# Performance work log

Hardware: AMD Instinct MI355X
Metric: run time of the kernel (lower is better)

The kernel has to match this reference:

```python
import jax, jax.numpy as jnp
import numpy as np

N_NODES = 50000
N_EDGES = 800000
VOCAB = 4096          # node_emb_size
EMB_DIM = 128         # node_emb_dim
HIDDEN = 128          # hidden_dim -> layer1 out = 2*HIDDEN
N_POS = 1024


def gcn_conv(h, edge_index, W, b, n):
    """PyG GCNConv: lin -> add self loops -> sym-normalized scatter-add -> +bias."""
    h = h @ W                                   # [N, out]
    row, col = edge_index[0], edge_index[1]     # source, target
    loop = jnp.arange(n)
    row = jnp.concatenate([row, loop])
    col = jnp.concatenate([col, loop])
    deg = jax.ops.segment_sum(jnp.ones(row.shape[0], dtype=h.dtype), col, num_segments=n)
    dinv = jnp.where(deg > 0, jax.lax.rsqrt(deg), 0.0)
    norm = dinv[row] * dinv[col]                # [E+N]
    msg = h[row] * norm[:, None]                # gather + scale
    return jax.ops.segment_sum(msg, col, num_segments=n) + b


def setup_inputs() -> dict:
    key = jax.random.key(0)
    ks = jax.random.split(key, 10)
    x = jax.random.randint(ks[0], (N_NODES, 1), 0, VOCAB)
    edge_index = jax.random.randint(ks[1], (2, N_EDGES), 0, N_NODES)
    x_position = jax.random.randint(ks[2], (N_POS,), 0, N_NODES)
    # Embedding init: normal(0, emb_dim^-0.5) per initialize_parameters
    emb = jax.random.normal(ks[3], (VOCAB, EMB_DIM), jnp.float32) * EMB_DIM ** -0.5
    # GCN / linear weights (glorot-ish)
    W1 = jax.random.normal(ks[4], (EMB_DIM, 2 * HIDDEN), jnp.float32) * (EMB_DIM ** -0.5)
    b1 = jnp.zeros((2 * HIDDEN,), jnp.float32)
    W2 = jax.random.normal(ks[5], (2 * HIDDEN, HIDDEN), jnp.float32) * ((2 * HIDDEN) ** -0.5)
    b2 = jnp.zeros((HIDDEN,), jnp.float32)
    Wc = jax.random.normal(ks[6], (HIDDEN, VOCAB), jnp.float32) * (HIDDEN ** -0.5)
    bc = jnp.zeros((VOCAB,), jnp.float32)
    return {"x": x, "edge_index": edge_index, "x_position": x_position,
            "emb": emb, "W1": W1, "b1": b1, "W2": W2, "b2": b2, "Wc": Wc, "bc": bc}


def reference(x, edge_index, x_position, emb, W1, b1, W2, b2, Wc, bc):
    n = x.shape[0]
    h = emb[x[:, 0]]                                   # Embedding + squeeze(1)
    h = jax.nn.relu(gcn_conv(h, edge_index, W1, b1, n))
    z = gcn_conv(h, edge_index, W2, b2, n)             # [N, HIDDEN]
    logits = z @ Wc + bc                               # classifier over all nodes
    # embedding stage: mean of classified rows at x_position, keep dim 0
    return jnp.mean(logits[x_position], axis=0, keepdims=True)  # [1, VOCAB]
```

## Files before the change

kernel.cpp:

```cpp
#include <hip/hip_runtime.h>

constexpr int EMB  = 128;
constexpr int H1D  = 256;
constexpr int H2D  = 128;
constexpr int VOC  = 4096;
constexpr int NSL  = 32;

__global__ void k_init(int* cnt, int* count, float* wsum, int* nflag, int* total, int n) {
    int i = blockIdx.x * blockDim.x + threadIdx.x;
    if (i < n) { cnt[i] = 0; count[i] = 0; }
    if (i < NSL * H1D) wsum[i] = 0.0f;
    if (i == 0) { *nflag = 0; *total = 0; }
}

__global__ void k_histcnt(const int* __restrict__ col, const int* __restrict__ xpos,
                          int* cnt, int* count, int ne, int np) {
    int e = blockIdx.x * blockDim.x + threadIdx.x;
    if (e < ne) atomicAdd(&cnt[col[e]], 1);
    if (e < np) atomicAdd(&count[xpos[e]], 1);
}

__global__ void k_waggE(const int* __restrict__ row, const int* __restrict__ col,
                        const int* __restrict__ count, const int* __restrict__ cnt,
                        float* wagg, int ne) {
    int e = blockIdx.x * blockDim.x + threadIdx.x;
    if (e < ne) {
        int c = col[e];
        int cc = count[c];
        if (cc > 0) {
            int r = row[e];
            float dc = rsqrtf((float)cnt[c] + 1.0f);
            float dr = rsqrtf((float)cnt[r] + 1.0f);
            atomicAdd(&wagg[r], (float)cc * dc * dr);
        }
    }
}

__global__ void k_alloc(float* wagg, const int* __restrict__ cnt,
                        const int* __restrict__ count,
                        int* needlist, int* nflag, int* total,
                        int* offs, int* cursor, int n) {
    int v = blockIdx.x * blockDim.x + threadIdx.x;
    int lane = threadIdx.x & 63;
    float wa = 0.0f;
    int cv = 0;
    bool need = false;
    if (v < n) {
        wa = wagg[v];
        int cc = count[v];
        cv = cnt[v];
        if (cc > 0) {
            float d2 = 1.0f / ((float)cv + 1.0f);
            wa += (float)cc * d2;
        }
        need = (wa > 0.0f);
        if (need) wagg[v] = wa;
    }
    int seg = need ? cv : 0;
    int incl = seg;
#pragma unroll
    for (int d = 1; d < 64; d <<= 1) {
        int t = __shfl_up(incl, d);
        if (lane >= d) incl += t;
    }
    int excl = incl - seg;
    int wave_total = __shfl(incl, 63);
    unsigned long long mask = __ballot(need);
    int rank = __popcll(mask & ((1ull << lane) - 1));
    int wcnt = __popcll(mask);
    int base_id = 0, base_off = 0;
    if (lane == 0) {
        if (wcnt > 0) base_id = atomicAdd(nflag, wcnt);
        if (wave_total > 0) base_off = atomicAdd(total, wave_total);
    }
    base_id  = __shfl(base_id, 0);
    base_off = __shfl(base_off, 0);
    if (need) {
        needlist[base_id + rank] = v;
        int o = base_off + excl;
        offs[v] = o;
        cursor[v] = o;
    }
}

__global__ void k_scatter(const int* __restrict__ row, const int* __restrict__ col,
                          const float* __restrict__ wagg, const int* __restrict__ x,
                          const int* __restrict__ cnt,
                          int* cursor, int* srowx, float* srowd, int ne) {
    int e = blockIdx.x * blockDim.x + threadIdx.x;
    if (e < ne) {
        int c = col[e];
        if (wagg[c] > 0.0f) {
            int r = row[e];
            int pos = atomicAdd(&cursor[c], 1);
            srowx[pos] = x[r];
            srowd[pos] = rsqrtf((float)cnt[r] + 1.0f);
        }
    }
}

constexpr int RPB = 16;
__global__ void k_embW1(const float* __restrict__ emb, const float* __restrict__ W1,
                        float* __restrict__ embW1) {
    __shared__ float er[RPB][EMB];
    int t = threadIdx.x;
    int r0 = blockIdx.x * RPB;
    for (int i = t; i < RPB * EMB; i += 256) {
        er[i / EMB][i % EMB] = emb[(size_t)r0 * EMB + i];
    }
    __syncthreads();
    float acc[RPB];
#pragma unroll
    for (int rr = 0; rr < RPB; rr++) acc[rr] = 0.0f;
    for (int k = 0; k < EMB; k++) {
        float w = W1[k * H1D + t];
#pragma unroll
        for (int rr = 0; rr < RPB; rr++) acc[rr] += er[rr][k] * w;
    }
#pragma unroll
    for (int rr = 0; rr < RPB; rr++) {
        embW1[(size_t)(r0 + rr) * H1D + t] = acc[rr];
    }
}

__global__ void k_fconv(const int* __restrict__ needlist, const int* __restrict__ nneed_p,
                        const float* __restrict__ wagg, const int* __restrict__ x,
                        const int* __restrict__ srowx, const float* __restrict__ srowd,
                        const int* __restrict__ offs, const int* __restrict__ cnt,
                        const float* __restrict__ embW1, const float* __restrict__ b1,
                        float* __restrict__ wsum) {
    int lane = threadIdx.x & 63;
    int wib  = threadIdx.x >> 6;
    int wid  = blockIdx.x * (blockDim.x >> 6) + wib;
    int nw   = gridDim.x * (blockDim.x >> 6);
    int nn   = *nneed_p;
    const float4* __restrict__ ew = (const float4*)embW1;
    float4 bfrag = ((const float4*)b1)[lane];
    float4 acc2 = {0.0f, 0.0f, 0.0f, 0.0f};

    for (int i = wid; i < nn; i += nw) {
        int v = needlist[i];
        int cv = cnt[v];
        float dv = rsqrtf((float)cv + 1.0f);
        float wa = wagg[v];
        float4 s = ew[(size_t)x[v] * 64 + lane];
        float w0 = dv * dv;
        float4 acc;
        acc.x = bfrag.x + w0 * s.x;
        acc.y = bfrag.y + w0 * s.y;
        acc.z = bfrag.z + w0 * s.z;
        acc.w = bfrag.w + w0 * s.w;
        int start = offs[v], m = cv;
        for (int base = 0; base < m; base += 64) {
            int mm = min(64, m - base);
            int xr = 0; float wr = 0.0f;
            if (lane < mm) {
                xr = srowx[start + base + lane];
                wr = srowd[start + base + lane] * dv;
            }
            int e = 0;
            for (; e + 4 <= mm; e += 4) {
                int i0 = __shfl(xr, e),     i1 = __shfl(xr, e + 1);
                int i2 = __shfl(xr, e + 2), i3 = __shfl(xr, e + 3);
                float q0 = __shfl(wr, e),     q1 = __shfl(wr, e + 1);
                float q2 = __shfl(wr, e + 2), q3 = __shfl(wr, e + 3);
                float4 t0 = ew[(size_t)i0 * 64 + lane];
                float4 t1 = ew[(size_t)i1 * 64 + lane];
                float4 t2 = ew[(size_t)i2 * 64 + lane];
                float4 t3 = ew[(size_t)i3 * 64 + lane];
                acc.x += q0 * t0.x + q1 * t1.x + q2 * t2.x + q3 * t3.x;
                acc.y += q0 * t0.y + q1 * t1.y + q2 * t2.y + q3 * t3.y;
                acc.z += q0 * t0.z + q1 * t1.z + q2 * t2.z + q3 * t3.z;
                acc.w += q0 * t0.w + q1 * t1.w + q2 * t2.w + q3 * t3.w;
            }
            for (; e < mm; e++) {
                int i0 = __shfl(xr, e);
                float q0 = __shfl(wr, e);
                float4 t0 = ew[(size_t)i0 * 64 + lane];
                acc.x += q0 * t0.x;
                acc.y += q0 * t0.y;
                acc.z += q0 * t0.z;
                acc.w += q0 * t0.w;
            }
        }
        acc2.x += wa * fmaxf(acc.x, 0.0f);
        acc2.y += wa * fmaxf(acc.y, 0.0f);
        acc2.z += wa * fmaxf(acc.z, 0.0f);
        acc2.w += wa * fmaxf(acc.w, 0.0f);
    }

    __shared__ float red[4][H1D];
    red[wib][4 * lane + 0] = acc2.x;
    red[wib][4 * lane + 1] = acc2.y;
    red[wib][4 * lane + 2] = acc2.z;
    red[wib][4 * lane + 3] = acc2.w;
    __syncthreads();
    int t = threadIdx.x;
    float ssum = red[0][t] + red[1][t] + red[2][t] + red[3][t];
    atomicAdd(&wsum[(blockIdx.x & (NSL - 1)) * H1D + t], ssum);
}

__global__ void k_zout(const float* __restrict__ wsum, const float* __restrict__ W2,
                       const float* __restrict__ b2, const float* __restrict__ Wc,
                       const float* __restrict__ bc, float* __restrict__ out,
                       float inv_np) {
    __shared__ float ws[H1D];
    __shared__ float z[H2D];
    int t = threadIdx.x;
    float s = 0.0f;
#pragma unroll
    for (int c = 0; c < NSL; c++) s += wsum[c * H1D + t];
    ws[t] = s;
    __syncthreads();
    if (t < H2D) {
        float acc = 0.0f;
#pragma unroll 8
        for (int k = 0; k < H1D; k++) acc += ws[k] * W2[k * H2D + t];
        z[t] = b2[t] + acc * inv_np;
    }
    __syncthreads();
    int c = blockIdx.x * blockDim.x + t;
    float acc = bc[c];
#pragma unroll 8
    for (int j = 0; j < H2D; j++) acc += z[j] * Wc[(size_t)j * VOC + c];
    out[c] = acc;
}

extern "C" void kernel_launch(void* const* d_in, const int* in_sizes, int n_in,
                              void* d_out, int out_size, void* d_ws, size_t ws_size,
                              hipStream_t stream) {
    const int n  = in_sizes[0];
    const int ne = in_sizes[1] / 2;
    const int np = in_sizes[2];

    const int*   x    = (const int*)d_in[0];
    const int*   ei   = (const int*)d_in[1];
    const int*   xpos = (const int*)d_in[2];
    const float* emb  = (const float*)d_in[3];
    const float* W1   = (const float*)d_in[4];
    const float* b1   = (const float*)d_in[5];
    const float* W2   = (const float*)d_in[6];
    const float* b2   = (const float*)d_in[7];
    const float* Wc   = (const float*)d_in[8];
    const float* bc   = (const float*)d_in[9];
    float*       out  = (float*)d_out;

    const int* row = ei;
    const int* col = ei + ne;

    char* p = (char*)d_ws;
    auto alloc = [&](size_t bytes) {
        char* r = p;
        p += (bytes + 255) & ~(size_t)255;
        return r;
    };
    int*   cnt      = (int*)alloc((size_t)n * 4);
    int*   offs     = (int*)alloc((size_t)n * 4);
    int*   cursor   = (int*)alloc((size_t)n * 4);
    int*   count    = (int*)alloc((size_t)n * 4);
    int*   needlist = (int*)alloc((size_t)n * 4);
    int*   srowx    = (int*)alloc((size_t)ne * 4);
    float* srowd    = (float*)alloc((size_t)ne * 4);
    int*   nflag    = (int*)alloc(256 * 4);
    int*   total    = (int*)alloc(256 * 4);
    float* wagg     = (float*)alloc((size_t)n * 4);
    float* embW1    = (float*)alloc((size_t)VOC * H1D * 4);
    float* wsum     = (float*)alloc((size_t)NSL * H1D * 4);

    const int nb  = (n + 255) / 256;
    const int neb = (ne + 255) / 256;

    hipMemsetAsync(wagg, 0, (size_t)n * 4, stream);
    k_init<<<nb, 256, 0, stream>>>(cnt, count, wsum, nflag, total, n);
    k_histcnt<<<neb, 256, 0, stream>>>(col, xpos, cnt, count, ne, np);
    k_waggE<<<neb, 256, 0, stream>>>(row, col, count, cnt, wagg, ne);
    k_alloc<<<nb, 256, 0, stream>>>(wagg, cnt, count, needlist, nflag, total, offs, cursor, n);
    k_scatter<<<neb, 256, 0, stream>>>(row, col, wagg, x, cnt, cursor, srowx, srowd, ne);
    k_embW1<<<VOC / RPB, 256, 0, stream>>>(emb, W1, embW1);
    k_fconv<<<2048, 256, 0, stream>>>(needlist, nflag, wagg, x, srowx, srowd, offs, cnt,
                                      embW1, b1, wsum);
    k_zout<<<VOC / 256, 256, 0, stream>>>(wsum, W2, b2, Wc, bc, out, 1.0f / (float)np);
}
```

Measured before the change: 198.9 us.

## Fold edge weight accumulation into scatter and mark needed rows with bitmap

```diff
diff --git a/kernel.cpp b/kernel.cpp
--- a/kernel.cpp
+++ b/kernel.cpp
@@ -6,55 +6,51 @@
 constexpr int VOC  = 4096;
 constexpr int NSL  = 32;
 
-__global__ void k_init(int* cnt, int* count, float* wsum, int* nflag, int* total, int n) {
+__global__ void k_init(int* cnt, int* count, unsigned int* needed, float* wagg,
+                       float* wsum, int* nflag, int* total, int n, int nwords) {
     int i = blockIdx.x * blockDim.x + threadIdx.x;
-    if (i < n) { cnt[i] = 0; count[i] = 0; }
+    if (i < n) { cnt[i] = 0; count[i] = 0; wagg[i] = 0.0f; }
+    if (i < nwords) needed[i] = 0u;
     if (i < NSL * H1D) wsum[i] = 0.0f;
     if (i == 0) { *nflag = 0; *total = 0; }
 }
 
-__global__ void k_histcnt(const int* __restrict__ col, const int* __restrict__ xpos,
-                          int* cnt, int* count, int ne, int np) {
-    int e = blockIdx.x * blockDim.x + threadIdx.x;
-    if (e < ne) atomicAdd(&cnt[col[e]], 1);
-    if (e < np) atomicAdd(&count[xpos[e]], 1);
-}
-
-__global__ void k_waggE(const int* __restrict__ row, const int* __restrict__ col,
-                        const int* __restrict__ count, const int* __restrict__ cnt,
-                        float* wagg, int ne) {
+__global__ void k_count(const int* __restrict__ xpos, int* count, int np) {
+    int p = blockIdx.x * blockDim.x + threadIdx.x;
+    if (p < np) atomicAdd(&count[xpos[p]], 1);
+}
+
+__global__ void k_hist(const int* __restrict__ row, const int* __restrict__ col,
+                       const int* __restrict__ count, int* cnt,
+                       unsigned int* needed, int ne) {
     int e = blockIdx.x * blockDim.x + threadIdx.x;
     if (e < ne) {
         int c = col[e];
-        int cc = count[c];
-        if (cc > 0) {
+        atomicAdd(&cnt[c], 1);
+        if (count[c] > 0) {
             int r = row[e];
-            float dc = rsqrtf((float)cnt[c] + 1.0f);
-            float dr = rsqrtf((float)cnt[r] + 1.0f);
-            atomicAdd(&wagg[r], (float)cc * dc * dr);
+            atomicOr(&needed[r >> 5], 1u << (r & 31));
         }
     }
 }
 
-__global__ void k_alloc(float* wagg, const int* __restrict__ cnt,
-                        const int* __restrict__ count,
+__global__ void k_alloc(const unsigned int* __restrict__ needed,
+                        const int* __restrict__ cnt, const int* __restrict__ count,
+                        float* wagg, int* needb,
                         int* needlist, int* nflag, int* total,
                         int* offs, int* cursor, int n) {
     int v = blockIdx.x * blockDim.x + threadIdx.x;
     int lane = threadIdx.x & 63;
-    float wa = 0.0f;
     int cv = 0;
     bool need = false;
     if (v < n) {
-        wa = wagg[v];
+        cv = cnt[v];
         int cc = count[v];
-        cv = cnt[v];
-        if (cc > 0) {
-            float d2 = 1.0f / ((float)cv + 1.0f);
-            wa += (float)cc * d2;
-        }
-        need = (wa > 0.0f);
-        if (need) wagg[v] = wa;
+        bool bit = (needed[v >> 5] >> (v & 31)) & 1u;
+        bool flag = (cc > 0);
+        need = bit || flag;
+        needb[v] = need ? 1 : 0;
+        if (flag) wagg[v] = (float)cc / ((float)cv + 1.0f);
     }
     int seg = need ? cv : 0;
     int incl = seg;
@@ -84,17 +80,23 @@
 }
 
 __global__ void k_scatter(const int* __restrict__ row, const int* __restrict__ col,
-                          const float* __restrict__ wagg, const int* __restrict__ x,
-                          const int* __restrict__ cnt,
-                          int* cursor, int* srowx, float* srowd, int ne) {
+                          const int* __restrict__ needb, const int* __restrict__ count,
+                          const int* __restrict__ x, const int* __restrict__ cnt,
+                          int* cursor, int* srowx, float* srowd, float* wagg, int ne) {
     int e = blockIdx.x * blockDim.x + threadIdx.x;
     if (e < ne) {
         int c = col[e];
-        if (wagg[c] > 0.0f) {
+        if (needb[c]) {
             int r = row[e];
             int pos = atomicAdd(&cursor[c], 1);
+            float dr = rsqrtf((float)cnt[r] + 1.0f);
             srowx[pos] = x[r];
-            srowd[pos] = rsqrtf((float)cnt[r] + 1.0f);
+            srowd[pos] = dr;
+            int cc = count[c];
+            if (cc > 0) {
+                float dc = rsqrtf((float)cnt[c] + 1.0f);
+                atomicAdd(&wagg[r], (float)cc * dc * dr);
+            }
         }
     }
 }
@@ -254,28 +256,32 @@
         p += (bytes + 255) & ~(size_t)255;
         return r;
     };
-    int*   cnt      = (int*)alloc((size_t)n * 4);
-    int*   offs     = (int*)alloc((size_t)n * 4);
-    int*   cursor   = (int*)alloc((size_t)n * 4);
-    int*   count    = (int*)alloc((size_t)n * 4);
-    int*   needlist = (int*)alloc((size_t)n * 4);
-    int*   srowx    = (int*)alloc((size_t)ne * 4);
-    float* srowd    = (float*)alloc((size_t)ne * 4);
-    int*   nflag    = (int*)alloc(256 * 4);
-    int*   total    = (int*)alloc(256 * 4);
-    float* wagg     = (float*)alloc((size_t)n * 4);
-    float* embW1    = (float*)alloc((size_t)VOC * H1D * 4);
-    float* wsum     = (float*)alloc((size_t)NSL * H1D * 4);
-
-    const int nb  = (n + 255) / 256;
-    const int neb = (ne + 255) / 256;
-
-    hipMemsetAsync(wagg, 0, (size_t)n * 4, stream);
-    k_init<<<nb, 256, 0, stream>>>(cnt, count, wsum, nflag, total, n);
-    k_histcnt<<<neb, 256, 0, stream>>>(col, xpos, cnt, count, ne, np);
-    k_waggE<<<neb, 256, 0, stream>>>(row, col, count, cnt, wagg, ne);
-    k_alloc<<<nb, 256, 0, stream>>>(wagg, cnt, count, needlist, nflag, total, offs, cursor, n);
-    k_scatter<<<neb, 256, 0, stream>>>(row, col, wagg, x, cnt, cursor, srowx, srowd, ne);
+    int*          cnt      = (int*)alloc((size_t)n * 4);
+    int*          offs     = (int*)alloc((size_t)n * 4);
+    int*          cursor   = (int*)alloc((size_t)n * 4);
+    int*          count    = (int*)alloc((size_t)n * 4);
+    int*          needb    = (int*)alloc((size_t)n * 4);
+    int*          needlist = (int*)alloc((size_t)n * 4);
+    unsigned int* needed   = (unsigned int*)alloc((size_t)((n + 31) / 32) * 4);
+    int*          srowx    = (int*)alloc((size_t)ne * 4);
+    float*        srowd    = (float*)alloc((size_t)ne * 4);
+    int*          nflag    = (int*)alloc(256 * 4);
+    int*          total    = (int*)alloc(256 * 4);
+    float*        wagg     = (float*)alloc((size_t)n * 4);
+    float*        embW1    = (float*)alloc((size_t)VOC * H1D * 4);
+    float*        wsum     = (float*)alloc((size_t)NSL * H1D * 4);
+
+    const int nb     = (n + 255) / 256;
+    const int neb    = (ne + 255) / 256;
+    const int nwords = (n + 31) / 32;
+
+    k_init<<<nb, 256, 0, stream>>>(cnt, count, needed, wagg, wsum, nflag, total, n, nwords);
+    k_count<<<(np + 255) / 256, 256, 0, stream>>>(xpos, count, np);
+    k_hist<<<neb, 256, 0, stream>>>(row, col, count, cnt, needed, ne);
+    k_alloc<<<nb, 256, 0, stream>>>(needed, cnt, count, wagg, needb,
+                                    needlist, nflag, total, offs, cursor, n);
+    k_scatter<<<neb, 256, 0, stream>>>(row, col, needb, count, x, cnt,
+                                       cursor, srowx, srowd, wagg, ne);
     k_embW1<<<VOC / RPB, 256, 0, stream>>>(emb, W1, embW1);
     k_fconv<<<2048, 256, 0, stream>>>(needlist, nflag, wagg, x, srowx, srowd, offs, cnt,
                                       embW1, b1, wsum);
```

Result: faster. 194.6 us (-2.2%).
